# Kernel optimization log

Measured on AMD Instinct MI355X. Metric: run time of the kernel, lower is better.

The kernel has to match this reference:

```python
import jax, jax.numpy as jnp
import numpy as np

B, S, D = 4, 8192, 1024

def log_g(x):
    # log of g(x): log(x + 0.5) for x >= 0, log(sigmoid(x)) = -softplus(-x) otherwise
    return jnp.where(x >= 0, jnp.log(jax.nn.relu(x) + 0.5), -jax.nn.softplus(-x))

def setup_inputs() -> dict:
    key = jax.random.key(0)
    k1, k2 = jax.random.split(key)
    x = jax.random.normal(k1, (B, S, D), dtype=jnp.float32)
    # Linear(dim, 3*dim, bias=False); stored as [dim, 3*dim] so y = x @ W
    W = jax.random.normal(k2, (D, 3 * D), dtype=jnp.float32) * (1.0 / np.sqrt(D))
    return {"x": x, "W": W}

def reference(x, W):
    # x: [B, S, D], W: [D, 3D]
    hW = jnp.einsum('bsd,de->bse', x, W)  # [B, S, 3D]
    hidden, f_gate, i_gate = jnp.split(hW, 3, axis=-1)

    # log-space normalized gates:
    # diff = softplus(-f) - softplus(-i); log_f' = -softplus(diff); log_i' = -softplus(-diff)
    diff = jax.nn.softplus(-f_gate) - jax.nn.softplus(-i_gate)
    log_f = -jax.nn.softplus(diff)
    log_i = -jax.nn.softplus(-diff)
    log_values = log_i + log_g(hidden)

    # Heinsen associative scan in log space (float32 internally)
    a_star = jnp.cumsum(log_f.astype(jnp.float32), axis=1)
    log_h0_plus_b_star = jax.lax.cumlogsumexp(log_values.astype(jnp.float32) - a_star, axis=1)
    log_h = a_star + log_h0_plus_b_star
    out = jnp.exp(log_h).astype(x.dtype)  # [B, S, D]
    return out
```

## Files before the change

kernel.cpp:

```cpp
#include <hip/hip_runtime.h>
#include <hip/hip_bf16.h>
#include <cstdint>
#include <cstddef>


#define BB 4
#define SS 8192
#define DD 1024
#define MM 32768
#define KK 1024
#define NN 3072
#define CHUNKS 256
#define CLEN 32
#define NCH 4096
#define NT 16

typedef __bf16 bf16;
typedef __bf16 bf16x2 __attribute__((ext_vector_type(2)));
typedef __bf16 bf16x4 __attribute__((ext_vector_type(4)));
typedef __bf16 bf16x8 __attribute__((ext_vector_type(8)));
typedef float f32x4 __attribute__((ext_vector_type(4)));

__device__ __forceinline__ void gload16(const bf16* g, bf16* l) {
  __builtin_amdgcn_global_load_lds(
      (const __attribute__((address_space(1))) unsigned int*)(const void*)g,
      (__attribute__((address_space(3))) unsigned int*)(void*)l,
      16, 0, 0);
}

__device__ __forceinline__ void gate2(float h, float f, float i,
                                      float& F, float& IG) {
  float P = __expf(fminf(-f, 80.f));
  float Q = __expf(fminf(-i, 80.f));
  float rZ = __builtin_amdgcn_rcpf(2.f + P + Q);
  float eh = __expf(fminf(-h, 80.f));
  float gh = (h >= 0.f) ? (h + 0.5f) : __builtin_amdgcn_rcpf(1.f + eh);
  F = (1.f + Q) * rZ;
  IG = (1.f + P) * gh * rZ;
}

__device__ __forceinline__ float laddexp(float a, float b) {
  float m = fmaxf(a, b);
  return m + __logf(1.f + __expf(fminf(a, b) - m));
}
__device__ __forceinline__ void comb(float& A, float& V, float Ac, float Vc) {
  V = laddexp(V + Ac, Vc);
  A += Ac;
}

__global__ __launch_bounds__(256) void k_cvt_x(const float4* __restrict__ x,
                                               bf16x4* __restrict__ xb) {
  int i = blockIdx.x * 256 + threadIdx.x;
  float4 v = x[i];
  bf16x4 o;
  o[0] = (bf16)v.x; o[1] = (bf16)v.y; o[2] = (bf16)v.z; o[3] = (bf16)v.w;
  xb[i] = o;
}

__global__ __launch_bounds__(256) void k_cvt_wt(const float* __restrict__ W,
                                                bf16* __restrict__ Wt) {
  __shared__ float tile[32][33];
  int n0 = blockIdx.x * 32, k0 = blockIdx.y * 32;
  int tx = threadIdx.x, ty = threadIdx.y;
#pragma unroll
  for (int i = 0; i < 32; i += 8)
    tile[ty + i][tx] = W[(size_t)(k0 + ty + i) * NN + n0 + tx];
  __syncthreads();
#pragma unroll
  for (int i = 0; i < 32; i += 8)
    Wt[(size_t)(n0 + ty + i) * KK + k0 + tx] = (bf16)tile[tx][ty + i];
}

__global__ __launch_bounds__(512, 2) void k_gemm(const bf16* __restrict__ A,
                                                 const bf16* __restrict__ Bt,
                                                 bf16* __restrict__ C) {
  __shared__ __align__(16) bf16 sm[65536];
  const int tid = threadIdx.x;
  const int lane = tid & 63;
  const int w = tid >> 6;
  const int wm = w >> 2;
  const int wn = w & 3;
  const int c16 = lane & 15;
  const int l4 = lane >> 4;

  int bid = blockIdx.x;
  int swz = (bid & 7) * 192 + (bid >> 3);
  int mT = swz / 12;
  int nT = swz - mT * 12;
  const int mBase = mT * 256, nBase = nT * 256;

  const int sr = tid >> 3;
  const int scol = ((tid & 7) ^ (sr & 7)) * 8;
  const bf16* gA = A + (size_t)(mBase + sr) * KK + scol;
  const bf16* gB = Bt + (size_t)(nBase + sr) * KK + scol;
  const int ld = tid * 8;

  const int sw8 = c16 & 7;
  const int sx0 = (l4 ^ sw8) * 8;
  const int sx1 = ((l4 + 4) ^ sw8) * 8;
  const int aRow = (wm * 64 + c16) * 64;
  const int bRow = (wn * 32 + c16) * 64;

  f32x4 acc[2][2][4][2];
#pragma unroll
  for (int a = 0; a < 2; ++a)
#pragma unroll
    for (int b2 = 0; b2 < 2; ++b2)
#pragma unroll
      for (int m = 0; m < 4; ++m)
#pragma unroll
        for (int n = 0; n < 2; ++n)
          acc[a][b2][m][n] = (f32x4){0.f, 0.f, 0.f, 0.f};

#define STGA(h, L, bo, ko) \
  gload16(gA + (h) * 131072 + (L) * 65536 + (ko), \
          sm + (bo) + (h) * 8192 + (L) * 4096 + ld)
#define STGB(h, L, bo, ko) \
  gload16(gB + (h) * 131072 + (L) * 65536 + (ko), \
          sm + (bo) + 16384 + (h) * 8192 + (L) * 4096 + ld)
#define LDA(qm, AF)                                                     \
  _Pragma("unroll") for (int mi = 0; mi < 4; ++mi) {                    \
    const bf16* p_ = sm + buf + (qm) * 8192 + aRow + mi * 1024;         \
    AF[mi][0] = *(const bf16x8*)(p_ + sx0);                             \
    AF[mi][1] = *(const bf16x8*)(p_ + sx1);                             \
  }
#define LDB(qn, BF)                                                     \
  _Pragma("unroll") for (int ni = 0; ni < 2; ++ni) {                    \
    const bf16* p_ = sm + buf + 16384 + (qn) * 8192 + bRow + ni * 1024; \
    BF[ni][0] = *(const bf16x8*)(p_ + sx0);                             \
    BF[ni][1] = *(const bf16x8*)(p_ + sx1);                             \
  }
#define MFMAQ(qm, qn, AF, BF)                                             \
  __builtin_amdgcn_s_setprio(1);                                          \
  _Pragma("unroll") for (int mi = 0; mi < 4; ++mi)                        \
  _Pragma("unroll") for (int ni = 0; ni < 2; ++ni) {                      \
    acc[qm][qn][mi][ni] = __builtin_amdgcn_mfma_f32_16x16x32_bf16(        \
        AF[mi][0], BF[ni][0], acc[qm][qn][mi][ni], 0, 0, 0);              \
    acc[qm][qn][mi][ni] = __builtin_amdgcn_mfma_f32_16x16x32_bf16(        \
        AF[mi][1], BF[ni][1], acc[qm][qn][mi][ni], 0, 0, 0);              \
  }                                                                       \
  __builtin_amdgcn_s_setprio(0);
#define BAR asm volatile("s_barrier" ::: "memory")
#define VMC(n) asm volatile("s_waitcnt vmcnt(" #n ")" ::: "memory")

  STGA(0, 0, 0, 0); STGA(0, 1, 0, 0); STGB(0, 0, 0, 0); STGB(0, 1, 0, 0);
  STGA(1, 0, 0, 0); STGA(1, 1, 0, 0); STGB(1, 0, 0, 0); STGB(1, 1, 0, 0);
  VMC(4);
  BAR;

  bf16x8 afr[4][2], bfr0[2][2], bfr1[2][2];

  for (int t = 0; t < NT - 1; ++t) {
    const int buf = (t & 1) << 15;
    const int nb = buf ^ 32768;
    const int ko = (t + 1) * 64;
    LDA(0, afr); LDB(0, bfr0);
    STGA(0, 0, nb, ko); STGA(0, 1, nb, ko);
    STGB(0, 0, nb, ko); STGB(0, 1, nb, ko);
    VMC(4);
    BAR;
    MFMAQ(0, 0, afr, bfr0);
    BAR;
    LDB(1, bfr1);
    STGA(1, 0, nb, ko); STGA(1, 1, nb, ko);
    BAR;
    MFMAQ(0, 1, afr, bfr1);
    BAR;
    LDA(1, afr);
    STGB(1, 0, nb, ko); STGB(1, 1, nb, ko);
    BAR;
    MFMAQ(1, 1, afr, bfr1);
    BAR;
    VMC(4);
    BAR;
    MFMAQ(1, 0, afr, bfr0);
    BAR;
  }
  {
    const int buf = 32768;
    LDA(0, afr); LDB(0, bfr0);
    VMC(0);
    BAR;
    MFMAQ(0, 0, afr, bfr0);
    BAR;
    LDB(1, bfr1);
    BAR;
    MFMAQ(0, 1, afr, bfr1);
    BAR;
    LDA(1, afr);
    BAR;
    MFMAQ(1, 1, afr, bfr1);
    BAR;
    MFMAQ(1, 0, afr, bfr0);
  }

  __syncthreads();
  const int rq = l4 * 4;
#pragma unroll
  for (int qm = 0; qm < 2; ++qm)
#pragma unroll
    for (int qn = 0; qn < 2; ++qn)
#pragma unroll
      for (int mi = 0; mi < 4; ++mi)
#pragma unroll
        for (int ni = 0; ni < 2; ++ni)
#pragma unroll
          for (int r = 0; r < 4; ++r) {
            int row = qm * 128 + wm * 64 + mi * 16 + rq + r;
            int col = (qn * 128 + wn * 32 + ni * 16 + c16) ^ ((row & 7) << 3);
            sm[row * 256 + col] = (bf16)acc[qm][qn][mi][ni][r];
          }
  __syncthreads();
#pragma unroll
  for (int p = 0; p < 16; ++p) {
    int row = p * 16 + (tid >> 5);
    int colL = (tid & 31) * 8;
    int col = colL ^ ((row & 7) << 3);
    bf16x8 v = *(const bf16x8*)(sm + row * 256 + col);
    *(bf16x8*)(C + (size_t)(mBase + row) * NN + nBase + colL) = v;
  }
#undef STGA
#undef STGB
#undef LDA
#undef LDB
#undef MFMAQ
#undef BAR
#undef VMC
}

__global__ __launch_bounds__(256, 6) void k_scan1(const bf16* __restrict__ hW,
                                                  float2* __restrict__ agg) {
  const int d0 = threadIdx.x * 4;
  const int b = blockIdx.y, c = blockIdx.z;
  const bf16* p = hW + (size_t)(b * SS + c * CLEN) * NN + d0;
  float Fp[4] = {1.f, 1.f, 1.f, 1.f};
  float v[4] = {0.f, 0.f, 0.f, 0.f};
  bf16x4 hh = *(const bf16x4*)(p);
  bf16x4 ff = *(const bf16x4*)(p + DD);
  bf16x4 ii = *(const bf16x4*)(p + 2 * DD);
#pragma unroll 4
  for (int j = 0; j < CLEN - 1; ++j) {
    p += NN;
    bf16x4 hn = *(const bf16x4*)(p);
    bf16x4 fn = *(const bf16x4*)(p + DD);
    bf16x4 in2 = *(const bf16x4*)(p + 2 * DD);
#pragma unroll
    for (int e = 0; e < 4; ++e) {
      float F, IG;
      gate2((float)hh[e], (float)ff[e], (float)ii[e], F, IG);
      v[e] = fmaf(v[e], F, IG);
      Fp[e] *= F;
    }
    hh = hn; ff = fn; ii = in2;
  }
#pragma unroll
  for (int e = 0; e < 4; ++e) {
    float F, IG;
    gate2((float)hh[e], (float)ff[e], (float)ii[e], F, IG);
    v[e] = fmaf(v[e], F, IG);
    Fp[e] *= F;
  }
  const size_t ch = (size_t)b * DD + d0;
#pragma unroll
  for (int e = 0; e < 4; ++e)
    agg[(ch + e) * CHUNKS + c] =
        make_float2(__logf(fmaxf(Fp[e], 1e-37f)), __logf(fmaxf(v[e], 1e-37f)));
}

__global__ __launch_bounds__(256) void k_scan2(const float2* __restrict__ agg,
                                               float2* __restrict__ pre) {
  const int ch = blockIdx.x * 4 + (threadIdx.x >> 6);
  const int lane = threadIdx.x & 63;
  const float4* src = (const float4*)(agg + (size_t)ch * CHUNKS);
  float4 v0 = src[lane * 2];
  float4 v1 = src[lane * 2 + 1];
  float A = v0.x, V = v0.y;
  comb(A, V, v0.z, v0.w);
  comb(A, V, v1.x, v1.y);
  comb(A, V, v1.z, v1.w);
#pragma unroll
  for (int off = 1; off < 64; off <<= 1) {
    float Ao = __shfl_up(A, off);
    float Vo = __shfl_up(V, off);
    if (lane >= off) {
      V = laddexp(Vo + A, V);
      A = Ao + A;
    }
  }
  float exA = __shfl_up(A, 1);
  float exV = __shfl_up(V, 1);
  if (lane == 0) { exA = 0.f; exV = -1e30f; }
  float4 o0, o1;
  o0.x = exA; o0.y = exV;
  comb(exA, exV, v0.x, v0.y);
  o0.z = exA; o0.w = exV;
  comb(exA, exV, v0.z, v0.w);
  o1.x = exA; o1.y = exV;
  comb(exA, exV, v1.x, v1.y);
  o1.z = exA; o1.w = exV;
  float4* dst = (float4*)(pre + (size_t)ch * CHUNKS);
  dst[lane * 2] = o0;
  dst[lane * 2 + 1] = o1;
}

__global__ __launch_bounds__(256, 6) void k_scan3(const bf16* __restrict__ hW,
                                                  const float2* __restrict__ pre,
                                                  float* __restrict__ out) {
  const int d0 = threadIdx.x * 4;
  const int b = blockIdx.y, c = blockIdx.z;
  const bf16* p = hW + (size_t)(b * SS + c * CLEN) * NN + d0;
  float* o = out + (size_t)(b * SS + c * CLEN) * DD + d0;
  const size_t ch = (size_t)b * DD + d0;
  float v[4];
#pragma unroll
  for (int e = 0; e < 4; ++e)
    v[e] = __expf(pre[(ch + e) * CHUNKS + c].y);
  bf16x4 hh = *(const bf16x4*)(p);
  bf16x4 ff = *(const bf16x4*)(p + DD);
  bf16x4 ii = *(const bf16x4*)(p + 2 * DD);
#pragma unroll 4
  for (int j = 0; j < CLEN - 1; ++j) {
    p += NN;
    bf16x4 hn = *(const bf16x4*)(p);
    bf16x4 fn = *(const bf16x4*)(p + DD);
    bf16x4 in2 = *(const bf16x4*)(p + 2 * DD);
    float4 ov;
#pragma unroll
    for (int e = 0; e < 4; ++e) {
      float F, IG;
      gate2((float)hh[e], (float)ff[e], (float)ii[e], F, IG);
      v[e] = fmaf(v[e], F, IG);
    }
    ov.x = v[0]; ov.y = v[1]; ov.z = v[2]; ov.w = v[3];
    *(float4*)o = ov;
    o += DD;
    hh = hn; ff = fn; ii = in2;
  }
  float4 ov;
#pragma unroll
  for (int e = 0; e < 4; ++e) {
    float F, IG;
    gate2((float)hh[e], (float)ff[e], (float)ii[e], F, IG);
    v[e] = fmaf(v[e], F, IG);
  }
  ov.x = v[0]; ov.y = v[1]; ov.z = v[2]; ov.w = v[3];
  *(float4*)o = ov;
}

extern "C" void kernel_launch(void* const* d_in, const int* in_sizes, int n_in,
                              void* d_out, int out_size, void* d_ws,
                              size_t ws_size, hipStream_t stream) {
  const float* x = (const float*)d_in[0];
  const float* W = (const float*)d_in[1];
  float* out = (float*)d_out;
  char* ws = (char*)d_ws;

  const size_t wtB = (size_t)NN * KK * 2;
  const size_t xbB = (size_t)MM * KK * 2;
  const size_t aggB = (size_t)CHUNKS * NCH * sizeof(float2);
  bf16* Wt = (bf16*)ws;
  bf16* xb = (bf16*)(ws + wtB);
  bf16* hW = (bf16*)(ws + wtB + xbB);
  float2* agg = (float2*)(ws + wtB);
  float2* pre = (float2*)(ws + wtB + aggB);

  k_cvt_wt<<<dim3(NN / 32, KK / 32), dim3(32, 8), 0, stream>>>(W, Wt);
  k_cvt_x<<<dim3(MM * KK / 4 / 256), dim3(256), 0, stream>>>((const float4*)x,
                                                             (bf16x4*)xb);
  k_gemm<<<dim3((NN / 256) * (MM / 256)), 512, 0, stream>>>(xb, Wt, hW);
  k_scan1<<<dim3(1, BB, CHUNKS), 256, 0, stream>>>(hW, agg);
  k_scan2<<<dim3(NCH / 4), 256, 0, stream>>>(agg, pre);
  k_scan3<<<dim3(1, BB, CHUNKS), 256, 0, stream>>>(hW, pre, out);
}
```

Baseline: 533.6 us.

## Drop intra-iteration GEMM barriers and halve scan chunk length

```diff
diff --git a/kernel.cpp b/kernel.cpp
--- a/kernel.cpp
+++ b/kernel.cpp
@@ -10,8 +10,8 @@
 #define MM 32768
 #define KK 1024
 #define NN 3072
-#define CHUNKS 256
-#define CLEN 32
+#define CHUNKS 512
+#define CLEN 16
 #define NCH 4096
 #define NT 16
 
@@ -160,21 +160,15 @@
     VMC(4);
     BAR;
     MFMAQ(0, 0, afr, bfr0);
-    BAR;
     LDB(1, bfr1);
     STGA(1, 0, nb, ko); STGA(1, 1, nb, ko);
-    BAR;
     MFMAQ(0, 1, afr, bfr1);
-    BAR;
     LDA(1, afr);
     STGB(1, 0, nb, ko); STGB(1, 1, nb, ko);
-    BAR;
     MFMAQ(1, 1, afr, bfr1);
-    BAR;
     VMC(4);
     BAR;
     MFMAQ(1, 0, afr, bfr0);
-    BAR;
   }
   {
     const int buf = 32768;
@@ -182,15 +176,10 @@
     VMC(0);
     BAR;
     MFMAQ(0, 0, afr, bfr0);
-    BAR;
     LDB(1, bfr1);
-    BAR;
     MFMAQ(0, 1, afr, bfr1);
-    BAR;
     LDA(1, afr);
-    BAR;
     MFMAQ(1, 1, afr, bfr1);
-    BAR;
     MFMAQ(1, 0, afr, bfr0);
   }
 
@@ -272,12 +261,16 @@
   const int ch = blockIdx.x * 4 + (threadIdx.x >> 6);
   const int lane = threadIdx.x & 63;
   const float4* src = (const float4*)(agg + (size_t)ch * CHUNKS);
-  float4 v0 = src[lane * 2];
-  float4 v1 = src[lane * 2 + 1];
-  float A = v0.x, V = v0.y;
-  comb(A, V, v0.z, v0.w);
-  comb(A, V, v1.x, v1.y);
-  comb(A, V, v1.z, v1.w);
+  float4 v[4];
+#pragma unroll
+  for (int q = 0; q < 4; ++q) v[q] = src[lane * 4 + q];
+  float A = v[0].x, V = v[0].y;
+  comb(A, V, v[0].z, v[0].w);
+#pragma unroll
+  for (int q = 1; q < 4; ++q) {
+    comb(A, V, v[q].x, v[q].y);
+    comb(A, V, v[q].z, v[q].w);
+  }
 #pragma unroll
   for (int off = 1; off < 64; off <<= 1) {
     float Ao = __shfl_up(A, off);
@@ -290,17 +283,16 @@
   float exA = __shfl_up(A, 1);
   float exV = __shfl_up(V, 1);
   if (lane == 0) { exA = 0.f; exV = -1e30f; }
-  float4 o0, o1;
-  o0.x = exA; o0.y = exV;
-  comb(exA, exV, v0.x, v0.y);
-  o0.z = exA; o0.w = exV;
-  comb(exA, exV, v0.z, v0.w);
-  o1.x = exA; o1.y = exV;
-  comb(exA, exV, v1.x, v1.y);
-  o1.z = exA; o1.w = exV;
   float4* dst = (float4*)(pre + (size_t)ch * CHUNKS);
-  dst[lane * 2] = o0;
-  dst[lane * 2 + 1] = o1;
+#pragma unroll
+  for (int q = 0; q < 4; ++q) {
+    float4 o;
+    o.x = exA; o.y = exV;
+    comb(exA, exV, v[q].x, v[q].y);
+    o.z = exA; o.w = exV;
+    comb(exA, exV, v[q].z, v[q].w);
+    dst[lane * 4 + q] = o;
+  }
 }
 
 __global__ __launch_bounds__(256, 6) void k_scan3(const bf16* __restrict__ hW,
```

New measurement: 544.2 us. Within noise of the previous version (+2.0%).
